# Optimization experiments

Hardware: AMD Instinct MI355X
Metric: run time of the kernel (lower is better)

The kernel has to match this reference:

```python
import jax, jax.numpy as jnp
import numpy as np

K = 8  # in-edges per non-source node (forward direction)

def _mp_forward(y, src_local, pre_w, pre_b, upd_w, upd_b):
    # y: [L, P, D] node features by topological level; src_local: [L-1, P*K]
    L, P, D = y.shape
    # level 0 has no in-edges: builtin mean gives z = 0 -> y += relu(update(0)) = relu(b)
    y0 = jax.nn.relu(upd_b) + y[0]
    def step(y_prev, inp):
        src, y_init = inp
        msg = jax.nn.relu(y_prev[src] @ pre_w + pre_b)      # [P*K, D] gather + msg FNN
        z = msg.reshape(P, K, D).mean(axis=1)               # fn.mean reduce
        y_new = jax.nn.relu(z @ upd_w + upd_b) + y_init     # update + residual
        return y_new, y_new
    _, ys = jax.lax.scan(step, y0, (src_local, y[1:]))
    return jnp.concatenate([y0[None], ys], axis=0)

def _mp_reverse(y, src_local, pre_w, pre_b, upd_w, upd_b):
    # propagate along reversed edges, reverse topological order
    L, P, D = y.shape
    dst_local = jnp.repeat(jnp.arange(P), K)                # local dst of each fwd edge
    y_last = jax.nn.relu(upd_b) + y[-1]                     # sinks: z = 0
    def step(y_next, inp):
        src, y_init = inp
        msg = jax.nn.relu(y_next[dst_local] @ pre_w + pre_b)            # [P*K, D]
        z_sum = jax.ops.segment_sum(msg, src, num_segments=P)
        deg = jax.ops.segment_sum(jnp.ones((P * K,), msg.dtype), src, num_segments=P)
        z = z_sum / jnp.maximum(deg, 1.0)[:, None]          # mean; zero-deg -> 0
        y_new = jax.nn.relu(z @ upd_w + upd_b) + y_init
        return y_new, y_new
    _, ys = jax.lax.scan(step, y_last, (src_local, y[:-1]), reverse=True)
    return jnp.concatenate([ys, y_last[None]], axis=0)

def setup_inputs() -> dict:
    key = jax.random.key(0)
    ks = jax.random.split(key, 16)
    N, node_dim, D = 131072, 128, 128   # D = out_dim // 2
    L, P = 16, 8192
    s = 0.06
    return {
        "x": jax.random.normal(ks[0], (N, node_dim), jnp.float32),
        "src_local": jax.random.randint(ks[1], (L - 1, P * K), 0, P).astype(jnp.int32),
        "nt_w1": jax.random.normal(ks[2], (node_dim, node_dim), jnp.float32) * s,
        "nt_b1": jax.random.normal(ks[3], (node_dim,), jnp.float32) * s,
        "nt_w2": jax.random.normal(ks[4], (node_dim, D), jnp.float32) * s,
        "nt_b2": jax.random.normal(ks[5], (D,), jnp.float32) * s,
        "f_pre_w": jax.random.normal(ks[6], (D, D), jnp.float32) * s,
        "f_pre_b": jax.random.normal(ks[7], (D,), jnp.float32) * s,
        "f_upd_w": jax.random.normal(ks[8], (D, D), jnp.float32) * s,
        "f_upd_b": jax.random.normal(ks[9], (D,), jnp.float32) * s,
        "b_pre_w": jax.random.normal(ks[10], (D, D), jnp.float32) * s,
        "b_pre_b": jax.random.normal(ks[11], (D,), jnp.float32) * s,
        "b_upd_w": jax.random.normal(ks[12], (D, D), jnp.float32) * s,
        "b_upd_b": jax.random.normal(ks[13], (D,), jnp.float32) * s,
    }

def reference(x, src_local, nt_w1, nt_b1, nt_w2, nt_b2,
              f_pre_w, f_pre_b, f_upd_w, f_upd_b,
              b_pre_w, b_pre_b, b_upd_w, b_upd_b):
    Lm1, PK = src_local.shape
    P, L = PK // K, Lm1 + 1
    N = x.shape[0]
    # node_transform: FNN(node_dim, [node_dim], out_dim//2)
    h = jax.nn.relu(x @ nt_w1 + nt_b1) @ nt_w2 + nt_b2      # [N, D]
    y = h.reshape(L, P, -1)
    hf = _mp_forward(y, src_local, f_pre_w, f_pre_b, f_upd_w, f_upd_b).reshape(N, -1)
    hb = _mp_reverse(y, src_local, b_pre_w, b_pre_b, b_upd_w, b_upd_b).reshape(N, -1)
    return jnp.concatenate([hf, hb], axis=1)
```

## Files before the change

kernel.cpp:

```cpp
#include <hip/hip_runtime.h>
#include <cstddef>
#include <cstdint>

#define DD   128
#define PP   8192
#define KK   8
#define LLV  16
#define NN   131072
#define NE   65536
#define NLVL 15

typedef _Float16 h8 __attribute__((ext_vector_type(8)));
typedef _Float16 h4 __attribute__((ext_vector_type(4)));
typedef float f4v __attribute__((ext_vector_type(4)));

__device__ __forceinline__ float4 ld4(const float* p) { return *(const float4*)p; }
__device__ __forceinline__ void st4(float* p, float4 v) { *(float4*)p = v; }

__device__ __forceinline__ int swz(int row, int k) { return row * 128 + (k ^ ((row & 7) << 3)); }
__device__ __forceinline__ int uswz(int row, int c) { return row * 128 + (c ^ ((row & 7) << 2)); }

__device__ __forceinline__ void split_store(_Float16* ah, _Float16* al, int row, int k0, float4 v) {
  int o = swz(row, k0);
  h4 hi, lo;
  _Float16 t0 = (_Float16)v.x; hi[0] = t0; lo[0] = (_Float16)(v.x - (float)t0);
  _Float16 t1 = (_Float16)v.y; hi[1] = t1; lo[1] = (_Float16)(v.y - (float)t1);
  _Float16 t2 = (_Float16)v.z; hi[2] = t2; lo[2] = (_Float16)(v.z - (float)t2);
  _Float16 t3 = (_Float16)v.w; hi[3] = t3; lo[3] = (_Float16)(v.w - (float)t3);
  *(h4*)(ah + o) = hi;
  *(h4*)(al + o) = lo;
}

__device__ __forceinline__ void load_bfrags1(const _Float16* __restrict__ img, int t16, int lane,
                                             h8 Bh[4], h8 Bl[4]) {
#pragma unroll
  for (int ks = 0; ks < 4; ks++) {
    int o = ((t16 * 4 + ks) * 64 + lane) * 8;
    Bh[ks] = *(const h8*)(img + o);
    Bl[ks] = *(const h8*)(img + 16384 + o);
  }
}

__device__ __forceinline__ f4v gemm_rt(const _Float16* __restrict__ ah, const _Float16* __restrict__ al,
                                       const h8 Bh[4], const h8 Bl[4], int rbase, int lane) {
  int r16 = lane & 15, kb = lane >> 4;
  int arow = rbase + r16;
  h8 Ah[4], Al[4];
#pragma unroll
  for (int ks = 0; ks < 4; ks++) {
    int o = swz(arow, ks * 32 + kb * 8);
    Ah[ks] = *(const h8*)(ah + o);
    Al[ks] = *(const h8*)(al + o);
  }
  f4v a = {0.f, 0.f, 0.f, 0.f};
#pragma unroll
  for (int ks = 0; ks < 4; ks++) a = __builtin_amdgcn_mfma_f32_16x16x32_f16(Ah[ks], Bh[ks], a, 0, 0, 0);
#pragma unroll
  for (int ks = 0; ks < 4; ks++) a = __builtin_amdgcn_mfma_f32_16x16x32_f16(Al[ks], Bh[ks], a, 0, 0, 0);
#pragma unroll
  for (int ks = 0; ks < 4; ks++) a = __builtin_amdgcn_mfma_f32_16x16x32_f16(Ah[ks], Bl[ks], a, 0, 0, 0);
  return a;
}

__global__ __launch_bounds__(256) void prep_all(
    const float* __restrict__ w0, const float* __restrict__ w1,
    const float* __restrict__ w2, const float* __restrict__ w3,
    const float* __restrict__ w4, const float* __restrict__ w5,
    _Float16* __restrict__ img_base) {
  int mat = blockIdx.x >> 3;
  int g = (blockIdx.x & 7) * 256 + threadIdx.x;
  const float* w;
  switch (mat) {
    case 0: w = w0; break;
    case 1: w = w1; break;
    case 2: w = w2; break;
    case 3: w = w3; break;
    case 4: w = w4; break;
    default: w = w5; break;
  }
  _Float16* img = img_base + (size_t)mat * 32768;
  int t16 = g >> 8, ks = (g >> 6) & 3, lane = g & 63;
  int n = t16 * 16 + (lane & 15);
  int kb = ks * 32 + (lane >> 4) * 8;
  h8 hi, lo;
#pragma unroll
  for (int j = 0; j < 8; j++) {
    float v = w[(kb + j) * 128 + n];
    _Float16 h = (_Float16)v;
    hi[j] = h;
    lo[j] = (_Float16)(v - (float)h);
  }
  int o = ((t16 * 4 + ks) * 64 + lane) * 8;
  *(h8*)(img + o) = hi;
  *(h8*)(img + 16384 + o) = lo;
}

__global__ __launch_bounds__(512, 4) void nt_kernel(
    const float* __restrict__ x,
    const _Float16* __restrict__ w1img, const float* __restrict__ b1,
    const _Float16* __restrict__ w2img, const float* __restrict__ b2,
    float* __restrict__ hout) {
  __shared__ __align__(16) _Float16 asplit[16384];
  __shared__ __align__(16) float dbuf[8192];
  _Float16* ah = asplit;
  _Float16* al = asplit + 8192;
  int tid = threadIdx.x;
  int lane = tid & 63, wv = tid >> 6;
  int c4 = tid & 31, rg4 = (tid >> 5) * 4;
  size_t base = (size_t)blockIdx.x * 64;

  h8 Bh[4], Bl[4];
  load_bfrags1(w1img, wv, lane, Bh, Bl);

#pragma unroll
  for (int j = 0; j < 4; j++) {
    int s = tid + j * 512;
    float4 v = ((const float4*)(x + base * 128))[s];
    split_store(ah, al, s >> 5, (s & 31) * 4, v);
  }
  __syncthreads();

  f4v acc[4];
#pragma unroll
  for (int rt = 0; rt < 4; rt++) acc[rt] = gemm_rt(ah, al, Bh, Bl, rt * 16, lane);
  {
    int r16 = lane & 15, kb = lane >> 4;
    int col = wv * 16 + r16;
    float b = b1[col];
#pragma unroll
    for (int rt = 0; rt < 4; rt++)
#pragma unroll
      for (int r = 0; r < 4; r++)
        dbuf[uswz(rt * 16 + kb * 4 + r, col)] = fmaxf(acc[rt][r] + b, 0.f);
  }
  load_bfrags1(w2img, wv, lane, Bh, Bl);
  __syncthreads();

  float4 uu[4];
#pragma unroll
  for (int i = 0; i < 4; i++) uu[i] = *(const float4*)(dbuf + uswz(rg4 + i, c4 * 4));
#pragma unroll
  for (int i = 0; i < 4; i++) split_store(ah, al, rg4 + i, c4 * 4, uu[i]);
  __syncthreads();

#pragma unroll
  for (int rt = 0; rt < 4; rt++) acc[rt] = gemm_rt(ah, al, Bh, Bl, rt * 16, lane);
  {
    int r16 = lane & 15, kb = lane >> 4;
    int col = wv * 16 + r16;
    float b = b2[col];
#pragma unroll
    for (int rt = 0; rt < 4; rt++)
#pragma unroll
      for (int r = 0; r < 4; r++)
        dbuf[uswz(rt * 16 + kb * 4 + r, col)] = acc[rt][r] + b;
  }
  __syncthreads();
#pragma unroll
  for (int i = 0; i < 4; i++)
    st4(hout + (base + rg4 + i) * 128 + c4 * 4, *(const float4*)(dbuf + uswz(rg4 + i, c4 * 4)));
}

__global__ __launch_bounds__(256) void csr_count(const int* __restrict__ src_all,
                                                 int* __restrict__ deg) {
  int e = blockIdx.x * 256 + threadIdx.x;
  int l = e >> 16;
  int q = src_all[e];
  atomicAdd(&deg[l * PP + q], 1);
}

__global__ __launch_bounds__(256) void csr_scan(const int* __restrict__ deg,
                                                int* __restrict__ offs,
                                                int* __restrict__ cursor) {
  int l = blockIdx.x;
  int t = threadIdx.x;
  const int* d = deg + l * PP;
  __shared__ int ssum[256];
  int loc[32];
  int s = 0;
#pragma unroll
  for (int j = 0; j < 32; j++) { loc[j] = d[t * 32 + j]; s += loc[j]; }
  ssum[t] = s;
  __syncthreads();
  for (int off = 1; off < 256; off <<= 1) {
    int v = (t >= off) ? ssum[t - off] : 0;
    __syncthreads();
    ssum[t] += v;
    __syncthreads();
  }
  int run = (t == 0) ? 0 : ssum[t - 1];
#pragma unroll
  for (int j = 0; j < 32; j++) {
    offs[l * (PP + 1) + t * 32 + j] = run;
    cursor[l * PP + t * 32 + j] = run;
    run += loc[j];
  }
  if (t == 255) offs[l * (PP + 1) + PP] = run;
}

__global__ __launch_bounds__(256) void csr_fill(const int* __restrict__ src_all,
                                                int* __restrict__ cursor,
                                                int* __restrict__ edges) {
  int e = blockIdx.x * 256 + threadIdx.x;
  int l = e >> 16;
  int q = src_all[e];
  int pos = atomicAdd(&cursor[l * PP + q], 1);
  edges[l * NE + pos] = (e & (NE - 1)) >> 3;
}

__global__ __launch_bounds__(512, 4) void mp_step(
    const float* __restrict__ h,
    const int* __restrict__ src_all,
    const int* __restrict__ offs,
    const int* __restrict__ edges,
    const _Float16* __restrict__ fw_upd_img, const float* __restrict__ fw_upd_b,
    const _Float16* __restrict__ fw_pre_img, const float* __restrict__ fw_pre_b,
    const _Float16* __restrict__ bw_upd_img, const float* __restrict__ bw_upd_b,
    const _Float16* __restrict__ bw_pre_img, const float* __restrict__ bw_pre_b,
    const float* __restrict__ mf_in, float* __restrict__ mf_out,
    const float* __restrict__ mb_in, float* __restrict__ mb_out,
    float* __restrict__ out, int step) {
  __shared__ __align__(16) _Float16 asplit[8192];
  __shared__ __align__(16) float dbuf[4096];
  _Float16* ah = asplit;
  _Float16* al = asplit + 4096;
  int tid = threadIdx.x;
  int lane = tid & 63, wv = tid >> 6;
  int c4 = tid & 31, rg2 = (tid >> 5) * 2;
  bool is_fwd = blockIdx.x < 256;
  int tile = (blockIdx.x & 255) * 32;
  int level = is_fwd ? step : 15 - step;
  const _Float16* upd_img = is_fwd ? fw_upd_img : bw_upd_img;
  const float* upd_b = is_fwd ? fw_upd_b : bw_upd_b;
  const _Float16* pre_img = is_fwd ? fw_pre_img : bw_pre_img;
  const float* pre_b = is_fwd ? fw_pre_b : bw_pre_b;
  const float* m_in  = is_fwd ? mf_in : mb_in;
  float* m_out       = is_fwd ? mf_out : mb_out;
  bool has_gather = (step > 0);
  bool has_mout   = (step < 15);
  int col_off = is_fwd ? 0 : 128;

  h8 Bh[4], Bl[4];
  load_bfrags1(upd_img, wv, lane, Bh, Bl);

  if (has_gather) {
    if (is_fwd) {
      const int* src = src_all + (step - 1) * NE;
#pragma unroll
      for (int i = 0; i < 2; i++) {
        int r = rg2 + i;
        int p = tile + r;
        float4 v[8];
#pragma unroll
        for (int k = 0; k < 8; k++) {
          int s = src[p * 8 + k];
          v[k] = ld4(m_in + (size_t)s * 128 + c4 * 4);
        }
        float4 a;
        a.x = ((v[0].x + v[1].x) + (v[2].x + v[3].x)) + ((v[4].x + v[5].x) + (v[6].x + v[7].x));
        a.y = ((v[0].y + v[1].y) + (v[2].y + v[3].y)) + ((v[4].y + v[5].y) + (v[6].y + v[7].y));
        a.z = ((v[0].z + v[1].z) + (v[2].z + v[3].z)) + ((v[4].z + v[5].z) + (v[6].z + v[7].z));
        a.w = ((v[0].w + v[1].w) + (v[2].w + v[3].w)) + ((v[4].w + v[5].w) + (v[6].w + v[7].w));
        a.x *= 0.125f; a.y *= 0.125f; a.z *= 0.125f; a.w *= 0.125f;
        split_store(ah, al, r, c4 * 4, a);
      }
    } else {
      const int* off_l = offs + level * (PP + 1);
      const int* ep = edges + level * NE;
#pragma unroll
      for (int i = 0; i < 2; i++) {
        int r = rg2 + i;
        int q = tile + r;
        int e0 = off_l[q], e1 = off_l[q + 1];
        float4 a = {0.f, 0.f, 0.f, 0.f};
        int idx = e0;
        for (; idx + 4 <= e1; idx += 4) {
          int p0 = ep[idx], p1 = ep[idx + 1], p2 = ep[idx + 2], p3 = ep[idx + 3];
          float4 v0 = ld4(m_in + (size_t)p0 * 128 + c4 * 4);
          float4 v1 = ld4(m_in + (size_t)p1 * 128 + c4 * 4);
          float4 v2 = ld4(m_in + (size_t)p2 * 128 + c4 * 4);
          float4 v3 = ld4(m_in + (size_t)p3 * 128 + c4 * 4);
          a.x += (v0.x + v1.x) + (v2.x + v3.x);
          a.y += (v0.y + v1.y) + (v2.y + v3.y);
          a.z += (v0.z + v1.z) + (v2.z + v3.z);
          a.w += (v0.w + v1.w) + (v2.w + v3.w);
        }
        for (; idx < e1; idx++) {
          int p = ep[idx];
          float4 v = ld4(m_in + (size_t)p * 128 + c4 * 4);
          a.x += v.x; a.y += v.y; a.z += v.z; a.w += v.w;
        }
        float inv = (e1 > e0) ? 1.0f / (float)(e1 - e0) : 0.f;
        a.x *= inv; a.y *= inv; a.z *= inv; a.w *= inv;
        split_store(ah, al, r, c4 * 4, a);
      }
    }
  } else {
    float4 z = {0.f, 0.f, 0.f, 0.f};
#pragma unroll
    for (int i = 0; i < 2; i++) split_store(ah, al, rg2 + i, c4 * 4, z);
  }
  __syncthreads();

  f4v acc[2];
#pragma unroll
  for (int rt = 0; rt < 2; rt++) acc[rt] = gemm_rt(ah, al, Bh, Bl, rt * 16, lane);
  {
    int r16 = lane & 15, kb = lane >> 4;
    int col = wv * 16 + r16;
    float b = upd_b[col];
#pragma unroll
    for (int rt = 0; rt < 2; rt++)
#pragma unroll
      for (int r = 0; r < 4; r++)
        dbuf[uswz(rt * 16 + kb * 4 + r, col)] = fmaxf(acc[rt][r] + b, 0.f);
  }
  if (has_mout) load_bfrags1(pre_img, wv, lane, Bh, Bl);
  __syncthreads();

  float4 u[2];
#pragma unroll
  for (int i = 0; i < 2; i++) {
    int r = rg2 + i;
    int n = level * PP + tile + r;
    float4 uv = *(const float4*)(dbuf + uswz(r, c4 * 4));
    float4 res = ld4(h + (size_t)n * 128 + c4 * 4);
    u[i].x = uv.x + res.x;
    u[i].y = uv.y + res.y;
    u[i].z = uv.z + res.z;
    u[i].w = uv.w + res.w;
    st4(out + (size_t)n * 256 + col_off + c4 * 4, u[i]);
  }

  if (has_mout) {
#pragma unroll
    for (int i = 0; i < 2; i++) split_store(ah, al, rg2 + i, c4 * 4, u[i]);
    __syncthreads();
#pragma unroll
    for (int rt = 0; rt < 2; rt++) acc[rt] = gemm_rt(ah, al, Bh, Bl, rt * 16, lane);
    {
      int r16 = lane & 15, kb = lane >> 4;
      int col = wv * 16 + r16;
      float b = pre_b[col];
#pragma unroll
      for (int rt = 0; rt < 2; rt++)
#pragma unroll
        for (int r = 0; r < 4; r++)
          dbuf[uswz(rt * 16 + kb * 4 + r, col)] = fmaxf(acc[rt][r] + b, 0.f);
    }
    __syncthreads();
#pragma unroll
    for (int i = 0; i < 2; i++) {
      int r = rg2 + i;
      float4 m = *(const float4*)(dbuf + uswz(r, c4 * 4));
      st4(m_out + (size_t)(tile + r) * 128 + c4 * 4, m);
    }
  }
}

extern "C" void kernel_launch(void* const* d_in, const int* in_sizes, int n_in,
                              void* d_out, int out_size, void* d_ws, size_t ws_size,
                              hipStream_t stream) {
  const float* x      = (const float*)d_in[0];
  const int*   src    = (const int*)d_in[1];
  const float* nt_w1  = (const float*)d_in[2];
  const float* nt_b1  = (const float*)d_in[3];
  const float* nt_w2  = (const float*)d_in[4];
  const float* nt_b2  = (const float*)d_in[5];
  const float* f_pre_w = (const float*)d_in[6];
  const float* f_pre_b = (const float*)d_in[7];
  const float* f_upd_w = (const float*)d_in[8];
  const float* f_upd_b = (const float*)d_in[9];
  const float* b_pre_w = (const float*)d_in[10];
  const float* b_pre_b = (const float*)d_in[11];
  const float* b_upd_w = (const float*)d_in[12];
  const float* b_upd_b = (const float*)d_in[13];
  float* out = (float*)d_out;

  float* wsf = (float*)d_ws;
  float* h   = wsf;
  float* mf0 = h + (size_t)NN * DD;
  float* mf1 = mf0 + (size_t)PP * DD;
  float* mb0 = mf1 + (size_t)PP * DD;
  float* mb1 = mb0 + (size_t)PP * DD;
  int* deg    = (int*)(mb1 + (size_t)PP * DD);
  int* offs   = deg + NLVL * PP;
  int* cursor = offs + NLVL * (PP + 1);
  int* edges  = cursor + NLVL * PP;

  uintptr_t ip = (uintptr_t)(edges + (size_t)NLVL * NE);
  ip = (ip + 15) & ~(uintptr_t)15;
  _Float16* img = (_Float16*)ip;
  _Float16* i_ntw1 = img;
  _Float16* i_ntw2 = img + 32768;
  _Float16* i_fupd = img + 2 * 32768;
  _Float16* i_fpre = img + 3 * 32768;
  _Float16* i_bupd = img + 4 * 32768;
  _Float16* i_bpre = img + 5 * 32768;

  hipMemsetAsync(deg, 0, (size_t)NLVL * PP * sizeof(int), stream);
  prep_all<<<48, 256, 0, stream>>>(nt_w1, nt_w2, f_upd_w, f_pre_w, b_upd_w, b_pre_w, img);

  nt_kernel<<<NN / 64, 512, 0, stream>>>(x, i_ntw1, nt_b1, i_ntw2, nt_b2, h);
  csr_count<<<NLVL * NE / 256, 256, 0, stream>>>(src, deg);
  csr_scan<<<NLVL, 256, 0, stream>>>(deg, offs, cursor);
  csr_fill<<<NLVL * NE / 256, 256, 0, stream>>>(src, cursor, edges);

  for (int s = 0; s < 16; s++) {
    const float* mf_in = (s & 1) ? mf0 : mf1;
    float* mf_out      = (s & 1) ? mf1 : mf0;
    const float* mb_in = (s & 1) ? mb0 : mb1;
    float* mb_out      = (s & 1) ? mb1 : mb0;
    mp_step<<<512, 512, 0, stream>>>(h, src, offs, edges,
                                     i_fupd, f_upd_b, i_fpre, f_pre_b,
                                     i_bupd, b_upd_b, i_bpre, b_pre_b,
                                     mf_in, mf_out, mb_in, mb_out, out, s);
  }
}
```

Before: 578.4 us.

## Store intermediate messages in fp16 and skip the update GEMM at step zero

Message buffers between propagation steps are now stored and gathered as fp16 instead of fp32, which halves the bytes moved by the random-access gathers. Step zero now computes relu(bias) plus the residual directly, so the zero-input update GEMM and its barriers are skipped. The residual load is issued earlier, weight fragments are loaded per phase, and the node-transform launch is moved after the CSR build. Storing messages in fp16 loses precision relative to the reference.

```diff
diff --git a/kernel.cpp b/kernel.cpp
--- a/kernel.cpp
+++ b/kernel.cpp
@@ -217,8 +217,8 @@
     const _Float16* __restrict__ fw_pre_img, const float* __restrict__ fw_pre_b,
     const _Float16* __restrict__ bw_upd_img, const float* __restrict__ bw_upd_b,
     const _Float16* __restrict__ bw_pre_img, const float* __restrict__ bw_pre_b,
-    const float* __restrict__ mf_in, float* __restrict__ mf_out,
-    const float* __restrict__ mb_in, float* __restrict__ mb_out,
+    const _Float16* __restrict__ mf_in, _Float16* __restrict__ mf_out,
+    const _Float16* __restrict__ mb_in, _Float16* __restrict__ mb_out,
     float* __restrict__ out, int step) {
   __shared__ __align__(16) _Float16 asplit[8192];
   __shared__ __align__(16) float dbuf[4096];
@@ -234,33 +234,54 @@
   const float* upd_b = is_fwd ? fw_upd_b : bw_upd_b;
   const _Float16* pre_img = is_fwd ? fw_pre_img : bw_pre_img;
   const float* pre_b = is_fwd ? fw_pre_b : bw_pre_b;
-  const float* m_in  = is_fwd ? mf_in : mb_in;
-  float* m_out       = is_fwd ? mf_out : mb_out;
-  bool has_gather = (step > 0);
-  bool has_mout   = (step < 15);
+  const _Float16* m_in = is_fwd ? mf_in : mb_in;
+  _Float16* m_out      = is_fwd ? mf_out : mb_out;
+  bool has_mout = (step < 15);
   int col_off = is_fwd ? 0 : 128;
 
-  h8 Bh[4], Bl[4];
-  load_bfrags1(upd_img, wv, lane, Bh, Bl);
-
-  if (has_gather) {
+  float4 res[2];
+#pragma unroll
+  for (int i = 0; i < 2; i++) {
+    int n = level * PP + tile + rg2 + i;
+    res[i] = ld4(h + (size_t)n * 128 + c4 * 4);
+  }
+
+  float4 u[2];
+  if (step == 0) {
+    float4 bv = ld4(upd_b + c4 * 4);
+    float4 rb;
+    rb.x = fmaxf(bv.x, 0.f); rb.y = fmaxf(bv.y, 0.f);
+    rb.z = fmaxf(bv.z, 0.f); rb.w = fmaxf(bv.w, 0.f);
+#pragma unroll
+    for (int i = 0; i < 2; i++) {
+      u[i].x = rb.x + res[i].x; u[i].y = rb.y + res[i].y;
+      u[i].z = rb.z + res[i].z; u[i].w = rb.w + res[i].w;
+    }
+  } else {
+    h8 BhU[4], BlU[4];
+    load_bfrags1(upd_img, wv, lane, BhU, BlU);
+
     if (is_fwd) {
       const int* src = src_all + (step - 1) * NE;
 #pragma unroll
       for (int i = 0; i < 2; i++) {
         int r = rg2 + i;
         int p = tile + r;
-        float4 v[8];
+        h4 v[8];
 #pragma unroll
         for (int k = 0; k < 8; k++) {
-          int s = src[p * 8 + k];
-          v[k] = ld4(m_in + (size_t)s * 128 + c4 * 4);
+          int sidx = src[p * 8 + k];
+          v[k] = *(const h4*)(m_in + (size_t)sidx * 128 + c4 * 4);
         }
         float4 a;
-        a.x = ((v[0].x + v[1].x) + (v[2].x + v[3].x)) + ((v[4].x + v[5].x) + (v[6].x + v[7].x));
-        a.y = ((v[0].y + v[1].y) + (v[2].y + v[3].y)) + ((v[4].y + v[5].y) + (v[6].y + v[7].y));
-        a.z = ((v[0].z + v[1].z) + (v[2].z + v[3].z)) + ((v[4].z + v[5].z) + (v[6].z + v[7].z));
-        a.w = ((v[0].w + v[1].w) + (v[2].w + v[3].w)) + ((v[4].w + v[5].w) + (v[6].w + v[7].w));
+        a.x = (((float)v[0][0] + (float)v[1][0]) + ((float)v[2][0] + (float)v[3][0])) +
+              (((float)v[4][0] + (float)v[5][0]) + ((float)v[6][0] + (float)v[7][0]));
+        a.y = (((float)v[0][1] + (float)v[1][1]) + ((float)v[2][1] + (float)v[3][1])) +
+              (((float)v[4][1] + (float)v[5][1]) + ((float)v[6][1] + (float)v[7][1]));
+        a.z = (((float)v[0][2] + (float)v[1][2]) + ((float)v[2][2] + (float)v[3][2])) +
+              (((float)v[4][2] + (float)v[5][2]) + ((float)v[6][2] + (float)v[7][2]));
+        a.w = (((float)v[0][3] + (float)v[1][3]) + ((float)v[2][3] + (float)v[3][3])) +
+              (((float)v[4][3] + (float)v[5][3]) + ((float)v[6][3] + (float)v[7][3]));
         a.x *= 0.125f; a.y *= 0.125f; a.z *= 0.125f; a.w *= 0.125f;
         split_store(ah, al, r, c4 * 4, a);
       }
@@ -276,68 +297,68 @@
         int idx = e0;
         for (; idx + 4 <= e1; idx += 4) {
           int p0 = ep[idx], p1 = ep[idx + 1], p2 = ep[idx + 2], p3 = ep[idx + 3];
-          float4 v0 = ld4(m_in + (size_t)p0 * 128 + c4 * 4);
-          float4 v1 = ld4(m_in + (size_t)p1 * 128 + c4 * 4);
-          float4 v2 = ld4(m_in + (size_t)p2 * 128 + c4 * 4);
-          float4 v3 = ld4(m_in + (size_t)p3 * 128 + c4 * 4);
-          a.x += (v0.x + v1.x) + (v2.x + v3.x);
-          a.y += (v0.y + v1.y) + (v2.y + v3.y);
-          a.z += (v0.z + v1.z) + (v2.z + v3.z);
-          a.w += (v0.w + v1.w) + (v2.w + v3.w);
+          h4 v0 = *(const h4*)(m_in + (size_t)p0 * 128 + c4 * 4);
+          h4 v1 = *(const h4*)(m_in + (size_t)p1 * 128 + c4 * 4);
+          h4 v2 = *(const h4*)(m_in + (size_t)p2 * 128 + c4 * 4);
+          h4 v3 = *(const h4*)(m_in + (size_t)p3 * 128 + c4 * 4);
+          a.x += ((float)v0[0] + (float)v1[0]) + ((float)v2[0] + (float)v3[0]);
+          a.y += ((float)v0[1] + (float)v1[1]) + ((float)v2[1] + (float)v3[1]);
+          a.z += ((float)v0[2] + (float)v1[2]) + ((float)v2[2] + (float)v3[2]);
+          a.w += ((float)v0[3] + (float)v1[3]) + ((float)v2[3] + (float)v3[3]);
         }
         for (; idx < e1; idx++) {
           int p = ep[idx];
-          float4 v = ld4(m_in + (size_t)p * 128 + c4 * 4);
-          a.x += v.x; a.y += v.y; a.z += v.z; a.w += v.w;
+          h4 v = *(const h4*)(m_in + (size_t)p * 128 + c4 * 4);
+          a.x += (float)v[0]; a.y += (float)v[1]; a.z += (float)v[2]; a.w += (float)v[3];
         }
         float inv = (e1 > e0) ? 1.0f / (float)(e1 - e0) : 0.f;
         a.x *= inv; a.y *= inv; a.z *= inv; a.w *= inv;
         split_store(ah, al, r, c4 * 4, a);
       }
     }
-  } else {
-    float4 z = {0.f, 0.f, 0.f, 0.f};
-#pragma unroll
-    for (int i = 0; i < 2; i++) split_store(ah, al, rg2 + i, c4 * 4, z);
-  }
-  __syncthreads();
-
-  f4v acc[2];
-#pragma unroll
-  for (int rt = 0; rt < 2; rt++) acc[rt] = gemm_rt(ah, al, Bh, Bl, rt * 16, lane);
-  {
-    int r16 = lane & 15, kb = lane >> 4;
-    int col = wv * 16 + r16;
-    float b = upd_b[col];
-#pragma unroll
-    for (int rt = 0; rt < 2; rt++)
-#pragma unroll
-      for (int r = 0; r < 4; r++)
-        dbuf[uswz(rt * 16 + kb * 4 + r, col)] = fmaxf(acc[rt][r] + b, 0.f);
-  }
-  if (has_mout) load_bfrags1(pre_img, wv, lane, Bh, Bl);
-  __syncthreads();
-
-  float4 u[2];
+    __syncthreads();
+
+    f4v acc[2];
+#pragma unroll
+    for (int rt = 0; rt < 2; rt++) acc[rt] = gemm_rt(ah, al, BhU, BlU, rt * 16, lane);
+    {
+      int r16 = lane & 15, kb = lane >> 4;
+      int col = wv * 16 + r16;
+      float b = upd_b[col];
+#pragma unroll
+      for (int rt = 0; rt < 2; rt++)
+#pragma unroll
+        for (int r = 0; r < 4; r++)
+          dbuf[uswz(rt * 16 + kb * 4 + r, col)] = fmaxf(acc[rt][r] + b, 0.f);
+    }
+    __syncthreads();
+
+#pragma unroll
+    for (int i = 0; i < 2; i++) {
+      int r = rg2 + i;
+      float4 uv = *(const float4*)(dbuf + uswz(r, c4 * 4));
+      u[i].x = uv.x + res[i].x;
+      u[i].y = uv.y + res[i].y;
+      u[i].z = uv.z + res[i].z;
+      u[i].w = uv.w + res[i].w;
+    }
+  }
+
 #pragma unroll
   for (int i = 0; i < 2; i++) {
-    int r = rg2 + i;
-    int n = level * PP + tile + r;
-    float4 uv = *(const float4*)(dbuf + uswz(r, c4 * 4));
-    float4 res = ld4(h + (size_t)n * 128 + c4 * 4);
-    u[i].x = uv.x + res.x;
-    u[i].y = uv.y + res.y;
-    u[i].z = uv.z + res.z;
-    u[i].w = uv.w + res.w;
+    int n = level * PP + tile + rg2 + i;
     st4(out + (size_t)n * 256 + col_off + c4 * 4, u[i]);
   }
 
   if (has_mout) {
+    h8 BhP[4], BlP[4];
+    load_bfrags1(pre_img, wv, lane, BhP, BlP);
 #pragma unroll
     for (int i = 0; i < 2; i++) split_store(ah, al, rg2 + i, c4 * 4, u[i]);
     __syncthreads();
-#pragma unroll
-    for (int rt = 0; rt < 2; rt++) acc[rt] = gemm_rt(ah, al, Bh, Bl, rt * 16, lane);
+    f4v acc[2];
+#pragma unroll
+    for (int rt = 0; rt < 2; rt++) acc[rt] = gemm_rt(ah, al, BhP, BlP, rt * 16, lane);
     {
       int r16 = lane & 15, kb = lane >> 4;
       int col = wv * 16 + r16;
@@ -353,7 +374,10 @@
     for (int i = 0; i < 2; i++) {
       int r = rg2 + i;
       float4 m = *(const float4*)(dbuf + uswz(r, c4 * 4));
-      st4(m_out + (size_t)(tile + r) * 128 + c4 * 4, m);
+      h4 mh;
+      mh[0] = (_Float16)m.x; mh[1] = (_Float16)m.y;
+      mh[2] = (_Float16)m.z; mh[3] = (_Float16)m.w;
+      *(h4*)(m_out + (size_t)(tile + r) * 128 + c4 * 4) = mh;
     }
   }
 }
@@ -379,10 +403,10 @@
 
   float* wsf = (float*)d_ws;
   float* h   = wsf;
-  float* mf0 = h + (size_t)NN * DD;
-  float* mf1 = mf0 + (size_t)PP * DD;
-  float* mb0 = mf1 + (size_t)PP * DD;
-  float* mb1 = mb0 + (size_t)PP * DD;
+  _Float16* mf0 = (_Float16*)(h + (size_t)NN * DD);
+  _Float16* mf1 = mf0 + (size_t)PP * DD;
+  _Float16* mb0 = mf1 + (size_t)PP * DD;
+  _Float16* mb1 = mb0 + (size_t)PP * DD;
   int* deg    = (int*)(mb1 + (size_t)PP * DD);
   int* offs   = deg + NLVL * PP;
   int* cursor = offs + NLVL * (PP + 1);
@@ -401,16 +425,16 @@
   hipMemsetAsync(deg, 0, (size_t)NLVL * PP * sizeof(int), stream);
   prep_all<<<48, 256, 0, stream>>>(nt_w1, nt_w2, f_upd_w, f_pre_w, b_upd_w, b_pre_w, img);
 
-  nt_kernel<<<NN / 64, 512, 0, stream>>>(x, i_ntw1, nt_b1, i_ntw2, nt_b2, h);
   csr_count<<<NLVL * NE / 256, 256, 0, stream>>>(src, deg);
   csr_scan<<<NLVL, 256, 0, stream>>>(deg, offs, cursor);
   csr_fill<<<NLVL * NE / 256, 256, 0, stream>>>(src, cursor, edges);
+  nt_kernel<<<NN / 64, 512, 0, stream>>>(x, i_ntw1, nt_b1, i_ntw2, nt_b2, h);
 
   for (int s = 0; s < 16; s++) {
-    const float* mf_in = (s & 1) ? mf0 : mf1;
-    float* mf_out      = (s & 1) ? mf1 : mf0;
-    const float* mb_in = (s & 1) ? mb0 : mb1;
-    float* mb_out      = (s & 1) ? mb1 : mb0;
+    const _Float16* mf_in = (s & 1) ? mf0 : mf1;
+    _Float16* mf_out      = (s & 1) ? mf1 : mf0;
+    const _Float16* mb_in = (s & 1) ? mb0 : mb1;
+    _Float16* mb_out      = (s & 1) ? mb1 : mb0;
     mp_step<<<512, 512, 0, stream>>>(h, src, offs, edges,
                                      i_fupd, f_upd_b, i_fpre, f_pre_b,
                                      i_bupd, b_upd_b, i_bpre, b_pre_b,
```

Result: no change. 569.5 us (-1.5%).
